# Optimization experiments

Measured on AMD Instinct MI355X. Metric: run time of the kernel, lower is better.

The kernel has to match this reference:

```python
import jax, jax.numpy as jnp
import numpy as np


def _cosine_alpha_bar(T, s=0.008):
    x = np.linspace(0.0, T, T + 1)
    ac = np.cos((x / T + s) / (1.0 + s) * np.pi / 2.0) ** 2
    ac = ac / ac[0]
    betas = np.clip(1.0 - ac[1:] / ac[:-1], 1e-5, 0.999)
    return jnp.asarray(np.cumprod(1.0 - betas), dtype=jnp.float32)


def setup_inputs():
    B, T, C, D, L, NS = 16, 1024, 16, 256, 4, 1000
    ks = list(jax.random.split(jax.random.key(0), 64))
    def w(i, shape, fan):
        return jax.random.normal(ks[i], shape, dtype=jnp.float32) / np.sqrt(fan)
    half = D // 2
    nf = half // 2
    inp = {}
    inp['x'] = jax.random.normal(ks[0], (B, T, C), dtype=jnp.float32)
    inp['t'] = jax.random.randint(ks[1], (B,), 0, NS, dtype=jnp.int32)
    dt = jax.random.uniform(ks[2], (B, T), minval=5e-4, maxval=2e-3, dtype=jnp.float32)
    inp['timestamps'] = jnp.cumsum(dt, axis=1)
    inp['mask'] = (jax.random.uniform(ks[3], (B, T, C)) > 0.3).astype(jnp.float32)
    inp['noise'] = jax.random.normal(ks[4], (B, T, D), dtype=jnp.float32)
    inp['n_heads'] = 4
    inp['alpha_bar'] = _cosine_alpha_bar(NS)
    inp['W_enc'] = w(5, (2 * C, D), 2 * C); inp['b_enc'] = jnp.zeros((D,), jnp.float32)
    inp['te_freqs'] = jnp.exp(-jnp.arange(half, dtype=jnp.float32) * np.log(10000.0) / half)
    inp['W_temb'] = w(6, (D, D), D); inp['b_temb'] = jnp.zeros((D,), jnp.float32)
    inp['th_a'] = 0.1 * jax.random.normal(ks[7], (half,), dtype=jnp.float32)
    inp['th_b'] = 0.1 * jax.random.normal(ks[8], (half,), dtype=jnp.float32)
    inp['th_freqs'] = (jnp.exp(-jnp.linspace(0.0, np.log(10000.0 / 4.0), nf)) * (2.0 * np.pi / 4.0)).astype(jnp.float32)
    inp['W_film'] = w(9, (D, 2 * D), D); inp['b_film'] = jnp.zeros((2 * D,), jnp.float32)
    inp['gru_Wih'] = w(10, (D, 3 * D), D); inp['gru_Whh'] = w(11, (D, 3 * D), D)
    inp['gru_bih'] = jnp.zeros((3 * D,), jnp.float32); inp['gru_bhh'] = jnp.zeros((3 * D,), jnp.float32)
    inp['ode_W1'] = w(12, (D, D), D); inp['ode_b1'] = jnp.zeros((D,), jnp.float32)
    inp['ode_W2'] = w(13, (D, D), D); inp['ode_b2'] = jnp.zeros((D,), jnp.float32)
    inp['tr_Wqkv'] = w(14, (L, D, 3 * D), D); inp['tr_bqkv'] = jnp.zeros((L, 3 * D), jnp.float32)
    inp['tr_Wo'] = w(15, (L, D, D), D); inp['tr_bo'] = jnp.zeros((L, D), jnp.float32)
    inp['tr_ln1_w'] = jnp.ones((L, D), jnp.float32); inp['tr_ln1_b'] = jnp.zeros((L, D), jnp.float32)
    inp['tr_ln2_w'] = jnp.ones((L, D), jnp.float32); inp['tr_ln2_b'] = jnp.zeros((L, D), jnp.float32)
    inp['tr_W1'] = w(16, (L, D, 4 * D), D); inp['tr_b1'] = jnp.zeros((L, 4 * D), jnp.float32)
    inp['tr_W2'] = w(17, (L, 4 * D, D), 4 * D); inp['tr_b2'] = jnp.zeros((L, D), jnp.float32)
    inp['trn_w'] = jnp.ones((D,), jnp.float32); inp['trn_b'] = jnp.zeros((D,), jnp.float32)
    return inp


def _ln(u, w_, b_):
    m = u.mean(-1, keepdims=True)
    v = u.var(-1, keepdims=True)
    return (u - m) / jnp.sqrt(v + 1e-5) * w_ + b_


def reference(x, t, timestamps, mask, noise, n_heads, alpha_bar, W_enc, b_enc, te_freqs, W_temb, b_temb, th_a, th_b, th_freqs, W_film, b_film, gru_Wih, gru_Whh, gru_bih, gru_bhh, ode_W1, ode_b1, ode_W2, ode_b2, tr_Wqkv, tr_bqkv, tr_Wo, tr_bo, tr_ln1_w, tr_ln1_b, tr_ln2_w, tr_ln2_b, tr_W1, tr_b1, tr_W2, tr_b2, trn_w, trn_b):
    B, T, C = x.shape
    D = W_enc.shape[1]
    hd = D // n_heads
    # latent encode + forward diffusion
    z = jax.nn.relu(jnp.concatenate([x, mask], -1) @ W_enc + b_enc)  # (B,T,D)
    ab = alpha_bar[t][:, None, None]
    h = jnp.sqrt(ab) * z + jnp.sqrt(1.0 - ab) * noise
    # diffusion-step sinusoidal embedding
    targ = t.astype(jnp.float32)[:, None] * te_freqs[None, :]
    te = (jnp.concatenate([jnp.sin(targ), jnp.cos(targ)], -1) @ W_temb + b_temb)[:, None, :]
    # TimeHybridEncoding: odd dims ramp, even dims interleaved sin/cos
    ts = timestamps
    ramp = ts[..., None] * th_a + th_b                       # (B,T,D/2)
    phase = ts[..., None] * th_freqs                         # (B,T,D/4)
    sc = jnp.stack([jnp.sin(phase), jnp.cos(phase)], -1).reshape(B, T, -1)
    tm = jnp.zeros((B, T, D), x.dtype).at[..., 0::2].set(sc).at[..., 1::2].set(ramp)
    gamma, beta = jnp.split(jax.nn.silu(te) @ W_film + b_film, 2, -1)
    tm = (1.0 + gamma) * tm + beta
    h = h + te + tm
    # Jump-ODE encoder: RK4 between events + GRUCell jump, as a scan
    dts = jnp.concatenate([jnp.zeros((B, 1), x.dtype), ts[:, 1:] - ts[:, :-1]], 1)[..., None]  # (B,T,1); dt0=0 -> identity ODE step
    def odef(hh):
        return jnp.tanh(hh @ ode_W1 + ode_b1) @ ode_W2 + ode_b2
    def step(hh, inp):
        xt, dt = inp
        f1 = odef(hh)
        f2 = odef(hh + 0.5 * dt * f1)
        f3 = odef(hh + 0.5 * dt * f2)
        f4 = odef(hh + dt * f3)
        hh = hh + dt / 6.0 * (f1 + 2.0 * f2 + 2.0 * f3 + f4)
        gi = xt @ gru_Wih + gru_bih
        gh = hh @ gru_Whh + gru_bhh
        ir, iz, inn = jnp.split(gi, 3, -1)
        hr, hz, hn = jnp.split(gh, 3, -1)
        r = jax.nn.sigmoid(ir + hr)
        zg = jax.nn.sigmoid(iz + hz)
        n = jnp.tanh(inn + r * hn)
        hh = (1.0 - zg) * n + zg * hh
        return hh, hh
    _, Hs = jax.lax.scan(step, jnp.zeros((B, D), x.dtype), (jnp.swapaxes(h, 0, 1), jnp.swapaxes(dts, 0, 1)))
    Hseq = jnp.swapaxes(Hs, 0, 1)  # (B,T,D)
    # pre-norm causal transformer encoder (eval mode, relu FFN), final LayerNorm
    causal = jnp.triu(jnp.full((T, T), -jnp.inf, dtype=x.dtype), 1)
    Ht = Hseq
    for l in range(tr_Wqkv.shape[0]):
        u = _ln(Ht, tr_ln1_w[l], tr_ln1_b[l])
        q, k, v = jnp.split(u @ tr_Wqkv[l] + tr_bqkv[l], 3, -1)
        q = q.reshape(B, T, n_heads, hd).transpose(0, 2, 1, 3)
        k = k.reshape(B, T, n_heads, hd).transpose(0, 2, 1, 3)
        v = v.reshape(B, T, n_heads, hd).transpose(0, 2, 1, 3)
        att = jax.nn.softmax(jnp.einsum('bhqd,bhkd->bhqk', q, k) / np.sqrt(hd) + causal, axis=-1)
        o = jnp.einsum('bhqk,bhkd->bhqd', att, v).transpose(0, 2, 1, 3).reshape(B, T, D)
        Ht = Ht + o @ tr_Wo[l] + tr_bo[l]
        u2 = _ln(Ht, tr_ln2_w[l], tr_ln2_b[l])
        Ht = Ht + jax.nn.relu(u2 @ tr_W1[l] + tr_b1[l]) @ tr_W2[l] + tr_b2[l]
    Ht = _ln(Ht, trn_w, trn_b)
    return Hseq + Ht
```

## Files before the change

kernel.cpp:

```cpp
#include <hip/hip_runtime.h>

#define Bz  16
#define Tz  1024
#define Cz  16
#define Dz  256
#define NHz 4
#define HDz 64
#define Lz  4
#define MROWS (Bz*Tz)
#define QB  8

__device__ __forceinline__ float sigmoidf_(float x){ return 1.0f/(1.0f+__expf(-x)); }
__device__ __forceinline__ float tanh_(float x){
  float e = __expf(2.f*x);
  return 1.f - 2.f/(e + 1.f);
}

__device__ __forceinline__ float dot2f(uint a, uint b, float c){
  float d;
  asm("v_dot2_f32_f16 %0, %1, %2, %3" : "=v"(d) : "v"(a), "v"(b), "v"(c));
  return d;
}
__device__ __forceinline__ uint f2h2(float a, float b){
  union { _Float16 h[2]; uint u; } r;
  r.h[0] = (_Float16)a; r.h[1] = (_Float16)b;
  return r.u;
}

__device__ __forceinline__ float red8(float a){
  int x = __builtin_amdgcn_update_dpp(0, __float_as_int(a), 0xB1, 0xF, 0xF, true);
  a += __int_as_float(x);
  x = __builtin_amdgcn_update_dpp(0, __float_as_int(a), 0x4E, 0xF, 0xF, true);
  a += __int_as_float(x);
  a += __shfl_xor(a, 4);
  return a;
}

__global__ __launch_bounds__(256) void k_prep(
    const float* __restrict__ W1, const float* __restrict__ W2, const float* __restrict__ Whh,
    uint* __restrict__ W1L, uint* __restrict__ W2L, uint* __restrict__ WhL)
{
  int m = blockIdx.x*256 + threadIdx.x;
  if (m < 65536){
    const float* W = (m < 32768) ? W1 : W2;
    uint* out = (m < 32768) ? W1L : W2L;
    int mm = m & 32767;
    int q = mm >> 2, cc = mm & 3;
    int i = q >> 9, l = q & 511;
    int j4 = l >> 3, ks = l & 7;
    int kp = ks*16 + i;
    int c = j4*4 + cc;
    out[mm] = f2h2(W[(2*kp)*256 + c], W[(2*kp+1)*256 + c]);
  } else if (m < 65536 + 98304){
    int mm = m - 65536;
    int g = mm >> 15;
    int r = mm & 32767;
    int q = r >> 2, cc = r & 3;
    int i = q >> 9, l = q & 511;
    int j4 = l >> 3, ks = l & 7;
    int kp = ks*16 + i;
    int c = j4*4 + cc;
    WhL[mm] = f2h2(Whh[(2*kp)*768 + g*256 + c], Whh[(2*kp+1)*768 + g*256 + c]);
  }
}

__global__ __launch_bounds__(256) void k_batch_emb(
    const int* __restrict__ t, const float* __restrict__ te_freqs,
    const float* __restrict__ W_temb, const float* __restrict__ b_temb,
    const float* __restrict__ W_film, const float* __restrict__ b_film,
    float* __restrict__ te_out, float* __restrict__ gamma_out, float* __restrict__ beta_out)
{
  int b = blockIdx.x; int j = threadIdx.x;
  __shared__ float s[256];
  __shared__ float ste[256];
  float tf = (float)t[b];
  if (j < 128){
    float targ = tf * te_freqs[j];
    s[j]     = __sinf(targ);
    s[j+128] = __cosf(targ);
  }
  __syncthreads();
  float a0=0,a1=0,a2=0,a3=0;
  #pragma unroll 8
  for (int k=0;k<256;k+=4){
    a0 = fmaf(s[k+0], W_temb[(k+0)*256+j], a0);
    a1 = fmaf(s[k+1], W_temb[(k+1)*256+j], a1);
    a2 = fmaf(s[k+2], W_temb[(k+2)*256+j], a2);
    a3 = fmaf(s[k+3], W_temb[(k+3)*256+j], a3);
  }
  float te = (a0+a1)+(a2+a3) + b_temb[j];
  te_out[b*256+j] = te;
  ste[j] = te * sigmoidf_(te);
  __syncthreads();
  float g0=0,g1=0,h0=0,h1=0;
  #pragma unroll 8
  for (int k=0;k<256;k+=2){
    float v0 = ste[k+0], v1 = ste[k+1];
    g0 = fmaf(v0, W_film[(k+0)*512+j],     g0);
    g1 = fmaf(v1, W_film[(k+1)*512+j],     g1);
    h0 = fmaf(v0, W_film[(k+0)*512+256+j], h0);
    h1 = fmaf(v1, W_film[(k+1)*512+256+j], h1);
  }
  gamma_out[b*256+j] = g0+g1 + b_film[j];
  beta_out [b*256+j] = h0+h1 + b_film[256+j];
}

__global__ __launch_bounds__(256) void k_encode(
    const float* __restrict__ x, const float* __restrict__ mask, const float* __restrict__ noise,
    const int* __restrict__ t, const float* __restrict__ alpha_bar, const float* __restrict__ ts,
    const float* __restrict__ W_enc, const float* __restrict__ b_enc,
    const float* __restrict__ th_a, const float* __restrict__ th_b, const float* __restrict__ th_freqs,
    const float* __restrict__ te, const float* __restrict__ gamma, const float* __restrict__ beta,
    float* __restrict__ H0)
{
  int bt = blockIdx.x; int b = bt >> 10;
  int j = threadIdx.x;
  __shared__ float in[32];
  if (j < 16)      in[j] = x[bt*16 + j];
  else if (j < 32) in[j] = mask[bt*16 + (j-16)];
  __syncthreads();
  float acc = 0.f;
  #pragma unroll
  for (int k=0;k<32;k++) acc = fmaf(in[k], W_enc[k*256+j], acc);
  float z = fmaxf(acc + b_enc[j], 0.f);
  float ab = alpha_bar[t[b]];
  float h = sqrtf(ab)*z + sqrtf(1.f-ab)*noise[(size_t)bt*256 + j];
  float tsv = ts[bt];
  float tm;
  if (j & 1){
    int i = (j-1) >> 1;
    tm = fmaf(tsv, th_a[i], th_b[i]);
  } else {
    int m = j >> 2;
    float ph = tsv * th_freqs[m];
    tm = ((j & 3) == 0) ? __sinf(ph) : __cosf(ph);
  }
  tm = fmaf(1.f + gamma[b*256+j], tm, beta[b*256+j]);
  H0[(size_t)bt*256 + j] = h + te[b*256+j] + tm;
}

template<bool RELU, bool RES>
__global__ __launch_bounds__(256) void k_gemm(
    const float* __restrict__ A, const float* __restrict__ W,
    const float* __restrict__ bias, const float* __restrict__ Rp,
    float* __restrict__ Cp, int M, int N, int K)
{
  __shared__ float As[16][68];
  __shared__ float Bs[16][64];
  int bn = blockIdx.x * 64, bm = blockIdx.y * 64;
  int tid = threadIdx.x;
  int tx = tid & 15, ty = tid >> 4;
  float acc[4][4] = {};
  for (int k0=0; k0<K; k0+=16){
    #pragma unroll
    for (int i=0;i<4;i++){
      int idx = tid + i*256;
      int m = idx >> 4, kk = idx & 15;
      As[kk][m] = A[(size_t)(bm+m)*K + k0+kk];
    }
    #pragma unroll
    for (int i=0;i<4;i++){
      int idx = tid + i*256;
      int kk = idx >> 6, n = idx & 63;
      Bs[kk][n] = W[(size_t)(k0+kk)*N + bn+n];
    }
    __syncthreads();
    #pragma unroll
    for (int kk=0;kk<16;kk++){
      float a0=As[kk][ty*4+0], a1=As[kk][ty*4+1], a2=As[kk][ty*4+2], a3=As[kk][ty*4+3];
      float b0=Bs[kk][tx*4+0], b1=Bs[kk][tx*4+1], b2=Bs[kk][tx*4+2], b3=Bs[kk][tx*4+3];
      acc[0][0]=fmaf(a0,b0,acc[0][0]); acc[0][1]=fmaf(a0,b1,acc[0][1]); acc[0][2]=fmaf(a0,b2,acc[0][2]); acc[0][3]=fmaf(a0,b3,acc[0][3]);
      acc[1][0]=fmaf(a1,b0,acc[1][0]); acc[1][1]=fmaf(a1,b1,acc[1][1]); acc[1][2]=fmaf(a1,b2,acc[1][2]); acc[1][3]=fmaf(a1,b3,acc[1][3]);
      acc[2][0]=fmaf(a2,b0,acc[2][0]); acc[2][1]=fmaf(a2,b1,acc[2][1]); acc[2][2]=fmaf(a2,b2,acc[2][2]); acc[2][3]=fmaf(a2,b3,acc[2][3]);
      acc[3][0]=fmaf(a3,b0,acc[3][0]); acc[3][1]=fmaf(a3,b1,acc[3][1]); acc[3][2]=fmaf(a3,b2,acc[3][2]); acc[3][3]=fmaf(a3,b3,acc[3][3]);
    }
    __syncthreads();
  }
  #pragma unroll
  for (int i=0;i<4;i++){
    int row = bm + ty*4 + i;
    #pragma unroll
    for (int jj=0;jj<4;jj++){
      int col = bn + tx*4 + jj;
      float v = acc[i][jj] + bias[col];
      if (RELU) v = fmaxf(v, 0.f);
      if (RES)  v += Rp[(size_t)row*N + col];
      Cp[(size_t)row*N + col] = v;
    }
  }
}

#define SCAN_LDS_BYTES (131072 + 1280)

#define DOT4V(WV, VW) { uint4 _w = (WV); \
  a0 = dot2f(_w.x, VW, a0); a1 = dot2f(_w.y, VW, a1); \
  a2 = dot2f(_w.z, VW, a2); a3 = dot2f(_w.w, VW, a3); }

#define MV16L(VB) { \
  uint4 q0=(VB)[ks5+0], q1=(VB)[ks5+1], q2=(VB)[ks5+2], q3=(VB)[ks5+3]; \
  DOT4V(w1s[0*512+tid], q0.x)  DOT4V(w1s[1*512+tid], q0.y)  DOT4V(w1s[2*512+tid], q0.z)  DOT4V(w1s[3*512+tid], q0.w)  \
  DOT4V(w1s[4*512+tid], q1.x)  DOT4V(w1s[5*512+tid], q1.y)  DOT4V(w1s[6*512+tid], q1.z)  DOT4V(w1s[7*512+tid], q1.w)  \
  DOT4V(w1s[8*512+tid], q2.x)  DOT4V(w1s[9*512+tid], q2.y)  DOT4V(w1s[10*512+tid], q2.z) DOT4V(w1s[11*512+tid], q2.w) \
  DOT4V(w1s[12*512+tid], q3.x) DOT4V(w1s[13*512+tid], q3.y) DOT4V(w1s[14*512+tid], q3.z) DOT4V(w1s[15*512+tid], q3.w) }

#define MV16R(W, VB) { \
  uint4 q0=(VB)[ks5+0], q1=(VB)[ks5+1], q2=(VB)[ks5+2], q3=(VB)[ks5+3]; \
  DOT4V(W[0], q0.x)  DOT4V(W[1], q0.y)  DOT4V(W[2], q0.z)  DOT4V(W[3], q0.w)  \
  DOT4V(W[4], q1.x)  DOT4V(W[5], q1.y)  DOT4V(W[6], q1.z)  DOT4V(W[7], q1.w)  \
  DOT4V(W[8], q2.x)  DOT4V(W[9], q2.y)  DOT4V(W[10], q2.z) DOT4V(W[11], q2.w) \
  DOT4V(W[12], q3.x) DOT4V(W[13], q3.y) DOT4V(W[14], q3.z) DOT4V(W[15], q3.w) }

#define DOTG(WV, VV, g0,g1,g2,g3) \
  g0 = dot2f((WV).x, VV, g0); g1 = dot2f((WV).y, VV, g1); \
  g2 = dot2f((WV).z, VV, g2); g3 = dot2f((WV).w, VV, g3);

#define LDQ(BUF, PO, I0) { \
  BUF[0]=WhL4[(PO)+((I0)+0)*512+tid]; BUF[1]=WhL4[(PO)+((I0)+1)*512+tid]; \
  BUF[2]=WhL4[(PO)+((I0)+2)*512+tid]; BUF[3]=WhL4[(PO)+((I0)+3)*512+tid]; }

#define DOTQ(BUF, Q, g0,g1,g2,g3) { \
  DOTG(BUF[0], (Q).x, g0,g1,g2,g3) DOTG(BUF[1], (Q).y, g0,g1,g2,g3) \
  DOTG(BUF[2], (Q).z, g0,g1,g2,g3) DOTG(BUF[3], (Q).w, g0,g1,g2,g3) }

__global__ __launch_bounds__(512) void k_scan(
    const uint* __restrict__ W1Lg, const uint* __restrict__ W2Lg, const uint* __restrict__ WhLg,
    const float* __restrict__ GI, const float* __restrict__ ts,
    const float* __restrict__ b1, const float* __restrict__ b2,
    const float* __restrict__ bhh, float* __restrict__ Hseq, float* __restrict__ Ht)
{
  extern __shared__ __align__(16) char smem[];
  uint4* w1s = (uint4*)smem;
  uint*  v2  = (uint*)(smem + 131072);
  const int b = blockIdx.x, tid = threadIdx.x;
  const int j4 = tid >> 3, ks = tid & 7;
  const int ks5 = ks*5;
  const uint4* W1L4 = (const uint4*)W1Lg;
  const uint4* W2L4 = (const uint4*)W2Lg;
  const uint4* WhL4 = (const uint4*)WhLg;
  #pragma unroll
  for (int i=0;i<16;i++) w1s[i*512+tid] = W1L4[i*512+tid];
  uint4 w2r[16];
  #pragma unroll
  for (int i=0;i<16;i++) w2r[i] = W2L4[i*512 + tid];
  if (tid < 320) v2[tid] = 0u;
  const float4 b1v  = ((const float4*)b1)[j4];
  const float4 b2v  = ((const float4*)b2)[j4];
  const float4 bhrv = ((const float4*)bhh)[j4];
  const float4 bhzv = ((const float4*)bhh)[64 + j4];
  const float4 bhnv = ((const float4*)bhh)[128 + j4];
  const float* tsb = ts + b*Tz;
  const float* gib = GI + (size_t)b*Tz*768;
  float* hsq = Hseq + (size_t)b*Tz*256;
  float* htp = Ht   + (size_t)b*Tz*256;
  const int wdw = 2*j4;
  const int wslot = (wdw >> 4)*20 + (wdw & 15);
  float4 h = {0.f,0.f,0.f,0.f};
  int cur = 0;
  float tsnext = tsb[0];
  float tprev = 0.f;
  __syncthreads();

  for (int tt=0; tt<Tz; ++tt){
    float tcur = tsnext;
    tsnext = tsb[(tt+1 < Tz) ? tt+1 : Tz-1];
    float dt = tcur - tprev; if (tt == 0) dt = 0.f;
    tprev = tcur;
    uint* bufA = v2 + (cur ? 160 : 0);
    uint* bufB = v2 + (cur ? 0 : 160);
    const uint4* vbA = (const uint4*)bufA;
    const uint4* vbB = (const uint4*)bufB;
    const float4 gi_r = *(const float4*)(gib + tt*768       + j4*4);
    const float4 gi_z = *(const float4*)(gib + tt*768 + 256 + j4*4);
    const float4 gi_n = *(const float4*)(gib + tt*768 + 512 + j4*4);
    uint4 whr[16];
    #pragma unroll
    for (int i=0;i<16;i++) whr[i] = WhL4[i*512 + tid];
    uint4 wA[4], wB[4];

    {
      float a0=0,a1=0,a2=0,a3=0;
      MV16L(vbA);
      a0=red8(a0); a1=red8(a1); a2=red8(a2); a3=red8(a3);
      float u0 = tanh_(a0+b1v.x), u1 = tanh_(a1+b1v.y);
      float u2 = tanh_(a2+b1v.z), u3 = tanh_(a3+b1v.w);
      if (ks == 0){
        uint2 pk; pk.x = f2h2(u0,u1); pk.y = f2h2(u2,u3);
        *(uint2*)(bufB + wslot) = pk;
      }
    }
    __syncthreads();
    float4 hn;
    LDQ(wA, 8192, 0)
    LDQ(wB, 8192, 4)
    {
      float a0=0,a1=0,a2=0,a3=0;
      MV16R(w2r, vbB);
      a0=red8(a0); a1=red8(a1); a2=red8(a2); a3=red8(a3);
      hn.x = fmaf(dt, a0+b2v.x, h.x);
      hn.y = fmaf(dt, a1+b2v.y, h.y);
      hn.z = fmaf(dt, a2+b2v.z, h.z);
      hn.w = fmaf(dt, a3+b2v.w, h.w);
      if (ks == 0){
        uint2 pk; pk.x = f2h2(hn.x,hn.y); pk.y = f2h2(hn.z,hn.w);
        *(uint2*)(bufA + wslot) = pk;
      }
    }
    __syncthreads();
    {
      uint4 q0=vbA[ks5+0], q1=vbA[ks5+1], q2=vbA[ks5+2], q3=vbA[ks5+3];
      float r0=0,r1=0,r2=0,r3=0, z0=0,z1=0,z2=0,z3=0, n0=0,n1=0,n2=0,n3=0;
      DOTG(whr[0], q0.x, r0,r1,r2,r3) DOTG(whr[1], q0.y, r0,r1,r2,r3)
      DOTG(whr[2], q0.z, r0,r1,r2,r3) DOTG(whr[3], q0.w, r0,r1,r2,r3)
      DOTG(whr[4], q1.x, r0,r1,r2,r3) DOTG(whr[5], q1.y, r0,r1,r2,r3)
      DOTG(whr[6], q1.z, r0,r1,r2,r3) DOTG(whr[7], q1.w, r0,r1,r2,r3)
      DOTG(whr[8], q2.x, r0,r1,r2,r3) DOTG(whr[9], q2.y, r0,r1,r2,r3)
      DOTG(whr[10],q2.z, r0,r1,r2,r3) DOTG(whr[11],q2.w, r0,r1,r2,r3)
      DOTG(whr[12],q3.x, r0,r1,r2,r3) DOTG(whr[13],q3.y, r0,r1,r2,r3)
      DOTG(whr[14],q3.z, r0,r1,r2,r3) DOTG(whr[15],q3.w, r0,r1,r2,r3)
      DOTQ(wA, q0, z0,z1,z2,z3)  LDQ(wA, 8192, 8)
      DOTQ(wB, q1, z0,z1,z2,z3)  LDQ(wB, 8192, 12)
      DOTQ(wA, q2, z0,z1,z2,z3)  LDQ(wA, 16384, 0)
      DOTQ(wB, q3, z0,z1,z2,z3)  LDQ(wB, 16384, 4)
      DOTQ(wA, q0, n0,n1,n2,n3)  LDQ(wA, 16384, 8)
      DOTQ(wB, q1, n0,n1,n2,n3)  LDQ(wB, 16384, 12)
      DOTQ(wA, q2, n0,n1,n2,n3)
      DOTQ(wB, q3, n0,n1,n2,n3)
      r0=red8(r0); r1=red8(r1); r2=red8(r2); r3=red8(r3);
      z0=red8(z0); z1=red8(z1); z2=red8(z2); z3=red8(z3);
      n0=red8(n0); n1=red8(n1); n2=red8(n2); n3=red8(n3);
      float gr0 = sigmoidf_(gi_r.x + r0 + bhrv.x);
      float gr1 = sigmoidf_(gi_r.y + r1 + bhrv.y);
      float gr2 = sigmoidf_(gi_r.z + r2 + bhrv.z);
      float gr3 = sigmoidf_(gi_r.w + r3 + bhrv.w);
      float gz0 = sigmoidf_(gi_z.x + z0 + bhzv.x);
      float gz1 = sigmoidf_(gi_z.y + z1 + bhzv.y);
      float gz2 = sigmoidf_(gi_z.z + z2 + bhzv.z);
      float gz3 = sigmoidf_(gi_z.w + z3 + bhzv.w);
      float gn0 = tanh_(gi_n.x + gr0*(n0 + bhnv.x));
      float gn1 = tanh_(gi_n.y + gr1*(n1 + bhnv.y));
      float gn2 = tanh_(gi_n.z + gr2*(n2 + bhnv.z));
      float gn3 = tanh_(gi_n.w + gr3*(n3 + bhnv.w));
      h.x = fmaf(gz0, hn.x - gn0, gn0);
      h.y = fmaf(gz1, hn.y - gn1, gn1);
      h.z = fmaf(gz2, hn.z - gn2, gn2);
      h.w = fmaf(gz3, hn.w - gn3, gn3);
      if (ks == 0){
        uint2 pk; pk.x = f2h2(h.x,h.y); pk.y = f2h2(h.z,h.w);
        *(uint2*)(bufB + wslot) = pk;
        *(float4*)(hsq + tt*256 + j4*4) = h;
        *(float4*)(htp + tt*256 + j4*4) = h;
      }
    }
    cur ^= 1;
    __syncthreads();
  }
}

__global__ __launch_bounds__(256) void k_attn(const float* __restrict__ QKV, float* __restrict__ O)
{
  int qb = blockIdx.x & (Tz/QB - 1);
  int bh = blockIdx.x / (Tz/QB);
  int b = bh >> 2, h = bh & 3;
  __shared__ uint Q2[QB][32];
  __shared__ float S[QB][Tz];
  __shared__ __align__(16) char kvbuf[64*68*4];
  __shared__ float rs[QB];
  uint  (*K2)[33] = (uint(*)[33])kvbuf;
  float (*Vs)[68] = (float(*)[68])kvbuf;
  int tid = threadIdx.x;
  const float* base = QKV + (size_t)b*Tz*768;
  for (int i = tid; i < QB*16; i += 256){
    int q = i >> 4, c = i & 15;
    const float4 v = *(const float4*)&base[(size_t)(qb*QB+q)*768 + h*64 + c*4];
    Q2[q][c*2]   = f2h2(v.x*0.125f, v.y*0.125f);
    Q2[q][c*2+1] = f2h2(v.z*0.125f, v.w*0.125f);
  }
  __syncthreads();
  int kmax = qb*QB + QB;
  int nkt = (kmax + 63) >> 6;
  int q = tid >> 5, i0 = tid & 31;
  int qg = qb*QB + q;
  for (int kt=0; kt<nkt; ++kt){
    for (int i=tid; i<64*16; i+=256){
      int r=i>>4, c=i&15;
      const float4 v = *(const float4*)&base[(size_t)(kt*64+r)*768 + 256 + h*64 + c*4];
      K2[r][c*2]   = f2h2(v.x, v.y);
      K2[r][c*2+1] = f2h2(v.z, v.w);
    }
    __syncthreads();
    float a0=0.f, a1=0.f;
    #pragma unroll 8
    for (int dp=0; dp<32; ++dp){
      uint qv = Q2[q][dp];
      a0 = dot2f(K2[i0][dp],    qv, a0);
      a1 = dot2f(K2[i0+32][dp], qv, a1);
    }
    int k0g = kt*64 + i0, k1g = k0g + 32;
    S[q][kt*64+i0]    = (k0g <= qg) ? a0 : -1e30f;
    S[q][kt*64+i0+32] = (k1g <= qg) ? a1 : -1e30f;
    __syncthreads();
  }
  int NK = nkt*64;
  float m = -1e30f;
  for (int kk=i0; kk<NK; kk+=32) m = fmaxf(m, S[q][kk]);
  #pragma unroll
  for (int o=16;o;o>>=1) m = fmaxf(m, __shfl_xor(m, o, 32));
  float sum = 0.f;
  for (int kk=i0; kk<NK; kk+=32){
    float p = __expf(S[q][kk] - m);
    S[q][kk] = p;
    sum += p;
  }
  #pragma unroll
  for (int o=16;o;o>>=1) sum += __shfl_xor(sum, o, 32);
  if (i0 == 0) rs[q] = 1.f/sum;
  int dq = tid & 15;
  int ks = (tid >> 4) & 1;
  float o0=0,o1=0,o2=0,o3=0;
  for (int kt=0; kt<nkt; ++kt){
    __syncthreads();
    for (int i=tid; i<64*16; i+=256){
      int r=i>>4, c=i&15;
      const float4 v = *(const float4*)&base[(size_t)(kt*64+r)*768 + 512 + h*64 + c*4];
      *(float4*)&Vs[r][c*4] = v;
    }
    __syncthreads();
    int kbase = kt*64;
    #pragma unroll 8
    for (int kk=ks; kk<64; kk+=2){
      float p = S[q][kbase+kk];
      const float4 vv = *(const float4*)&Vs[kk][dq*4];
      o0=fmaf(p,vv.x,o0); o1=fmaf(p,vv.y,o1); o2=fmaf(p,vv.z,o2); o3=fmaf(p,vv.w,o3);
    }
  }
  o0 += __shfl_xor(o0, 16); o1 += __shfl_xor(o1, 16);
  o2 += __shfl_xor(o2, 16); o3 += __shfl_xor(o3, 16);
  if (!(tid & 16)){
    float r = rs[q];
    size_t orow = ((size_t)b*Tz + qg)*256 + h*64 + dq*4;
    float4 ov = {o0*r, o1*r, o2*r, o3*r};
    *(float4*)&O[orow] = ov;
  }
}

template<bool FINAL>
__global__ __launch_bounds__(256) void k_ln(
    const float* __restrict__ in, const float* __restrict__ w, const float* __restrict__ bgain,
    const float* __restrict__ addv, float* __restrict__ out)
{
  int row  = blockIdx.x*4 + (threadIdx.x >> 6);
  int lane = threadIdx.x & 63;
  const float4 xv = ((const float4*)(in + (size_t)row*256))[lane];
  float s = xv.x + xv.y + xv.z + xv.w;
  #pragma unroll
  for (int o=32;o;o>>=1) s += __shfl_xor(s, o, 64);
  float mean = s * (1.f/256.f);
  float dx=xv.x-mean, dy=xv.y-mean, dz=xv.z-mean, dw=xv.w-mean;
  float qv = dx*dx + dy*dy + dz*dz + dw*dw;
  #pragma unroll
  for (int o=32;o;o>>=1) qv += __shfl_xor(qv, o, 64);
  float rstd = 1.f/sqrtf(qv*(1.f/256.f) + 1e-5f);
  const float4 wv = ((const float4*)w)[lane];
  const float4 bv = ((const float4*)bgain)[lane];
  float4 ov;
  ov.x = dx*rstd*wv.x + bv.x;
  ov.y = dy*rstd*wv.y + bv.y;
  ov.z = dz*rstd*wv.z + bv.z;
  ov.w = dw*rstd*wv.w + bv.w;
  if (FINAL){
    const float4 av = ((const float4*)(addv + (size_t)row*256))[lane];
    ov.x += av.x; ov.y += av.y; ov.z += av.z; ov.w += av.w;
  }
  ((float4*)(out + (size_t)row*256))[lane] = ov;
}

extern "C" void kernel_launch(void* const* d_in, const int* in_sizes, int n_in,
                              void* d_out, int out_size, void* d_ws, size_t ws_size,
                              hipStream_t stream)
{
  const float* x         = (const float*)d_in[0];
  const int*   t         = (const int*)  d_in[1];
  const float* ts        = (const float*)d_in[2];
  const float* mask      = (const float*)d_in[3];
  const float* noise     = (const float*)d_in[4];
  const float* alpha_bar = (const float*)d_in[6];
  const float* W_enc     = (const float*)d_in[7];
  const float* b_enc     = (const float*)d_in[8];
  const float* te_freqs  = (const float*)d_in[9];
  const float* W_temb    = (const float*)d_in[10];
  const float* b_temb    = (const float*)d_in[11];
  const float* th_a      = (const float*)d_in[12];
  const float* th_b      = (const float*)d_in[13];
  const float* th_freqs  = (const float*)d_in[14];
  const float* W_film    = (const float*)d_in[15];
  const float* b_film    = (const float*)d_in[16];
  const float* gru_Wih   = (const float*)d_in[17];
  const float* gru_Whh   = (const float*)d_in[18];
  const float* gru_bih   = (const float*)d_in[19];
  const float* gru_bhh   = (const float*)d_in[20];
  const float* ode_W1    = (const float*)d_in[21];
  const float* ode_b1    = (const float*)d_in[22];
  const float* ode_W2    = (const float*)d_in[23];
  const float* ode_b2    = (const float*)d_in[24];
  const float* tr_Wqkv   = (const float*)d_in[25];
  const float* tr_bqkv   = (const float*)d_in[26];
  const float* tr_Wo     = (const float*)d_in[27];
  const float* tr_bo     = (const float*)d_in[28];
  const float* tr_ln1_w  = (const float*)d_in[29];
  const float* tr_ln1_b  = (const float*)d_in[30];
  const float* tr_ln2_w  = (const float*)d_in[31];
  const float* tr_ln2_b  = (const float*)d_in[32];
  const float* tr_W1     = (const float*)d_in[33];
  const float* tr_b1     = (const float*)d_in[34];
  const float* tr_W2     = (const float*)d_in[35];
  const float* tr_b2     = (const float*)d_in[36];
  const float* trn_w     = (const float*)d_in[37];
  const float* trn_b     = (const float*)d_in[38];

  float* w = (float*)d_ws;
  float* te    = w;
  float* gamma = w + 4096;
  float* beta  = w + 8192;
  float* R1    = w + 12288;
  float* H0    = R1;
  float* GI    = R1 + 4*1024*1024;
  float* QKVb  = R1;
  float* F1    = R1;
  float* Hseq  = R1   + 16*1024*1024;
  float* Ht    = Hseq + 4*1024*1024;
  float* U     = Ht   + 4*1024*1024;
  float* O     = U    + 4*1024*1024;
  uint*  W1L   = (uint*)(O + 4*1024*1024);
  uint*  W2L   = W1L + 32768;
  uint*  WhL   = W2L + 32768;

  k_prep<<<640, 256, 0, stream>>>(ode_W1, ode_W2, gru_Whh, W1L, W2L, WhL);
  k_batch_emb<<<Bz, 256, 0, stream>>>(t, te_freqs, W_temb, b_temb, W_film, b_film, te, gamma, beta);
  k_encode<<<MROWS, 256, 0, stream>>>(x, mask, noise, t, alpha_bar, ts, W_enc, b_enc,
                                      th_a, th_b, th_freqs, te, gamma, beta, H0);
  k_gemm<false,false><<<dim3(768/64, MROWS/64), 256, 0, stream>>>(H0, gru_Wih, gru_bih, nullptr, GI, MROWS, 768, 256);

  hipFuncSetAttribute((const void*)k_scan, hipFuncAttributeMaxDynamicSharedMemorySize, SCAN_LDS_BYTES);
  k_scan<<<Bz, 512, SCAN_LDS_BYTES, stream>>>(W1L, W2L, WhL, GI, ts, ode_b1, ode_b2, gru_bhh, Hseq, Ht);

  for (int l=0; l<Lz; ++l){
    k_ln<false><<<MROWS/4, 256, 0, stream>>>(Ht, tr_ln1_w + l*256, tr_ln1_b + l*256, nullptr, U);
    k_gemm<false,false><<<dim3(768/64, MROWS/64), 256, 0, stream>>>(U, tr_Wqkv + (size_t)l*256*768, tr_bqkv + l*768, nullptr, QKVb, MROWS, 768, 256);
    k_attn<<<Bz*NHz*(Tz/QB), 256, 0, stream>>>(QKVb, O);
    k_gemm<false,true><<<dim3(256/64, MROWS/64), 256, 0, stream>>>(O, tr_Wo + (size_t)l*256*256, tr_bo + l*256, Ht, Ht, MROWS, 256, 256);
    k_ln<false><<<MROWS/4, 256, 0, stream>>>(Ht, tr_ln2_w + l*256, tr_ln2_b + l*256, nullptr, U);
    k_gemm<true,false><<<dim3(1024/64, MROWS/64), 256, 0, stream>>>(U, tr_W1 + (size_t)l*256*1024, tr_b1 + l*1024, nullptr, F1, MROWS, 1024, 256);
    k_gemm<false,true><<<dim3(256/64, MROWS/64), 256, 0, stream>>>(F1, tr_W2 + (size_t)l*1024*256, tr_b2 + l*256, Ht, Ht, MROWS, 256, 1024);
  }

  k_ln<true><<<MROWS/4, 256, 0, stream>>>(Ht, trn_w, trn_b, Hseq, (float*)d_out);
}
```

Before: 11.83 ms.

## Restructure GRU scan: DPP-only reduction, folded biases, earlier weight prefetch, drop Ht copy

Remaps the thread-to-(j4,ks) layout so the 8-lane reduction uses only DPP row operations instead of a cross-lane shuffle. It folds the r/z recurrent biases into the input-gate GEMM bias through a precomputed combined bias. The z and n weight loads are reissued earlier in larger batches to hide global latency behind the sync barriers. The scan no longer writes a duplicate Ht buffer, and the first transformer layer reads Hseq directly. The trade-off is higher register pressure, with launch bounds set to one block per CU.

```diff
diff --git a/kernel.cpp b/kernel.cpp
--- a/kernel.cpp
+++ b/kernel.cpp
@@ -32,13 +32,19 @@
   a += __int_as_float(x);
   x = __builtin_amdgcn_update_dpp(0, __float_as_int(a), 0x4E, 0xF, 0xF, true);
   a += __int_as_float(x);
-  a += __shfl_xor(a, 4);
+  x = __builtin_amdgcn_update_dpp(0, __float_as_int(a), 0x128, 0xF, 0xF, true);
+  a += __int_as_float(x);
   return a;
 }
+
+__device__ __forceinline__ int ks_of(int l){ return (l & 3) | ((l & 8) >> 1); }
+__device__ __forceinline__ int j4_of(int t){ return ((t & 4) >> 2) | ((t >> 4) << 1); }
 
 __global__ __launch_bounds__(256) void k_prep(
     const float* __restrict__ W1, const float* __restrict__ W2, const float* __restrict__ Whh,
-    uint* __restrict__ W1L, uint* __restrict__ W2L, uint* __restrict__ WhL)
+    const float* __restrict__ bih, const float* __restrict__ bhh,
+    uint* __restrict__ W1L, uint* __restrict__ W2L, uint* __restrict__ WhL,
+    float* __restrict__ biasC)
 {
   int m = blockIdx.x*256 + threadIdx.x;
   if (m < 65536){
@@ -47,7 +53,7 @@
     int mm = m & 32767;
     int q = mm >> 2, cc = mm & 3;
     int i = q >> 9, l = q & 511;
-    int j4 = l >> 3, ks = l & 7;
+    int ks = ks_of(l), j4 = j4_of(l);
     int kp = ks*16 + i;
     int c = j4*4 + cc;
     out[mm] = f2h2(W[(2*kp)*256 + c], W[(2*kp+1)*256 + c]);
@@ -57,10 +63,13 @@
     int r = mm & 32767;
     int q = r >> 2, cc = r & 3;
     int i = q >> 9, l = q & 511;
-    int j4 = l >> 3, ks = l & 7;
+    int ks = ks_of(l), j4 = j4_of(l);
     int kp = ks*16 + i;
     int c = j4*4 + cc;
     WhL[mm] = f2h2(Whh[(2*kp)*768 + g*256 + c], Whh[(2*kp+1)*768 + g*256 + c]);
+  } else if (m < 65536 + 98304 + 768){
+    int c = m - (65536 + 98304);
+    biasC[c] = bih[c] + ((c < 512) ? bhh[c] : 0.f);
   }
 }
 
@@ -214,25 +223,18 @@
   g0 = dot2f((WV).x, VV, g0); g1 = dot2f((WV).y, VV, g1); \
   g2 = dot2f((WV).z, VV, g2); g3 = dot2f((WV).w, VV, g3);
 
-#define LDQ(BUF, PO, I0) { \
-  BUF[0]=WhL4[(PO)+((I0)+0)*512+tid]; BUF[1]=WhL4[(PO)+((I0)+1)*512+tid]; \
-  BUF[2]=WhL4[(PO)+((I0)+2)*512+tid]; BUF[3]=WhL4[(PO)+((I0)+3)*512+tid]; }
-
-#define DOTQ(BUF, Q, g0,g1,g2,g3) { \
-  DOTG(BUF[0], (Q).x, g0,g1,g2,g3) DOTG(BUF[1], (Q).y, g0,g1,g2,g3) \
-  DOTG(BUF[2], (Q).z, g0,g1,g2,g3) DOTG(BUF[3], (Q).w, g0,g1,g2,g3) }
-
-__global__ __launch_bounds__(512) void k_scan(
+__global__ __launch_bounds__(512, 1) void k_scan(
     const uint* __restrict__ W1Lg, const uint* __restrict__ W2Lg, const uint* __restrict__ WhLg,
     const float* __restrict__ GI, const float* __restrict__ ts,
     const float* __restrict__ b1, const float* __restrict__ b2,
-    const float* __restrict__ bhh, float* __restrict__ Hseq, float* __restrict__ Ht)
+    const float* __restrict__ bhh, float* __restrict__ Hseq)
 {
   extern __shared__ __align__(16) char smem[];
   uint4* w1s = (uint4*)smem;
   uint*  v2  = (uint*)(smem + 131072);
   const int b = blockIdx.x, tid = threadIdx.x;
-  const int j4 = tid >> 3, ks = tid & 7;
+  const int ks = ks_of(tid & 63);
+  const int j4 = j4_of(tid);
   const int ks5 = ks*5;
   const uint4* W1L4 = (const uint4*)W1Lg;
   const uint4* W2L4 = (const uint4*)W2Lg;
@@ -245,37 +247,28 @@
   if (tid < 320) v2[tid] = 0u;
   const float4 b1v  = ((const float4*)b1)[j4];
   const float4 b2v  = ((const float4*)b2)[j4];
-  const float4 bhrv = ((const float4*)bhh)[j4];
-  const float4 bhzv = ((const float4*)bhh)[64 + j4];
   const float4 bhnv = ((const float4*)bhh)[128 + j4];
   const float* tsb = ts + b*Tz;
   const float* gib = GI + (size_t)b*Tz*768;
   float* hsq = Hseq + (size_t)b*Tz*256;
-  float* htp = Ht   + (size_t)b*Tz*256;
   const int wdw = 2*j4;
   const int wslot = (wdw >> 4)*20 + (wdw & 15);
   float4 h = {0.f,0.f,0.f,0.f};
   int cur = 0;
-  float tsnext = tsb[0];
   float tprev = 0.f;
   __syncthreads();
 
   for (int tt=0; tt<Tz; ++tt){
-    float tcur = tsnext;
-    tsnext = tsb[(tt+1 < Tz) ? tt+1 : Tz-1];
+    float tcur = tsb[tt];
     float dt = tcur - tprev; if (tt == 0) dt = 0.f;
     tprev = tcur;
     uint* bufA = v2 + (cur ? 160 : 0);
     uint* bufB = v2 + (cur ? 0 : 160);
     const uint4* vbA = (const uint4*)bufA;
     const uint4* vbB = (const uint4*)bufB;
-    const float4 gi_r = *(const float4*)(gib + tt*768       + j4*4);
-    const float4 gi_z = *(const float4*)(gib + tt*768 + 256 + j4*4);
-    const float4 gi_n = *(const float4*)(gib + tt*768 + 512 + j4*4);
     uint4 whr[16];
     #pragma unroll
     for (int i=0;i<16;i++) whr[i] = WhL4[i*512 + tid];
-    uint4 wA[4], wB[4];
 
     {
       float a0=0,a1=0,a2=0,a3=0;
@@ -288,10 +281,11 @@
         *(uint2*)(bufB + wslot) = pk;
       }
     }
+    uint4 wz1[8];
+    #pragma unroll
+    for (int i=0;i<8;i++) wz1[i] = WhL4[8192 + i*512 + tid];
     __syncthreads();
     float4 hn;
-    LDQ(wA, 8192, 0)
-    LDQ(wB, 8192, 4)
     {
       float a0=0,a1=0,a2=0,a3=0;
       MV16R(w2r, vbB);
@@ -305,10 +299,19 @@
         *(uint2*)(bufA + wslot) = pk;
       }
     }
+    uint4 wz2[8];
+    #pragma unroll
+    for (int i=0;i<8;i++) wz2[i] = WhL4[8192 + (8+i)*512 + tid];
+    const float4 gi_r = *(const float4*)(gib + tt*768       + j4*4);
+    const float4 gi_z = *(const float4*)(gib + tt*768 + 256 + j4*4);
+    const float4 gi_n = *(const float4*)(gib + tt*768 + 512 + j4*4);
     __syncthreads();
     {
       uint4 q0=vbA[ks5+0], q1=vbA[ks5+1], q2=vbA[ks5+2], q3=vbA[ks5+3];
       float r0=0,r1=0,r2=0,r3=0, z0=0,z1=0,z2=0,z3=0, n0=0,n1=0,n2=0,n3=0;
+      uint4 wn1[8];
+      #pragma unroll
+      for (int i=0;i<8;i++) wn1[i] = WhL4[16384 + i*512 + tid];
       DOTG(whr[0], q0.x, r0,r1,r2,r3) DOTG(whr[1], q0.y, r0,r1,r2,r3)
       DOTG(whr[2], q0.z, r0,r1,r2,r3) DOTG(whr[3], q0.w, r0,r1,r2,r3)
       DOTG(whr[4], q1.x, r0,r1,r2,r3) DOTG(whr[5], q1.y, r0,r1,r2,r3)
@@ -317,25 +320,36 @@
       DOTG(whr[10],q2.z, r0,r1,r2,r3) DOTG(whr[11],q2.w, r0,r1,r2,r3)
       DOTG(whr[12],q3.x, r0,r1,r2,r3) DOTG(whr[13],q3.y, r0,r1,r2,r3)
       DOTG(whr[14],q3.z, r0,r1,r2,r3) DOTG(whr[15],q3.w, r0,r1,r2,r3)
-      DOTQ(wA, q0, z0,z1,z2,z3)  LDQ(wA, 8192, 8)
-      DOTQ(wB, q1, z0,z1,z2,z3)  LDQ(wB, 8192, 12)
-      DOTQ(wA, q2, z0,z1,z2,z3)  LDQ(wA, 16384, 0)
-      DOTQ(wB, q3, z0,z1,z2,z3)  LDQ(wB, 16384, 4)
-      DOTQ(wA, q0, n0,n1,n2,n3)  LDQ(wA, 16384, 8)
-      DOTQ(wB, q1, n0,n1,n2,n3)  LDQ(wB, 16384, 12)
-      DOTQ(wA, q2, n0,n1,n2,n3)
-      DOTQ(wB, q3, n0,n1,n2,n3)
+      uint4 wn2[8];
+      #pragma unroll
+      for (int i=0;i<8;i++) wn2[i] = WhL4[16384 + (8+i)*512 + tid];
+      DOTG(wz1[0], q0.x, z0,z1,z2,z3) DOTG(wz1[1], q0.y, z0,z1,z2,z3)
+      DOTG(wz1[2], q0.z, z0,z1,z2,z3) DOTG(wz1[3], q0.w, z0,z1,z2,z3)
+      DOTG(wz1[4], q1.x, z0,z1,z2,z3) DOTG(wz1[5], q1.y, z0,z1,z2,z3)
+      DOTG(wz1[6], q1.z, z0,z1,z2,z3) DOTG(wz1[7], q1.w, z0,z1,z2,z3)
+      DOTG(wz2[0], q2.x, z0,z1,z2,z3) DOTG(wz2[1], q2.y, z0,z1,z2,z3)
+      DOTG(wz2[2], q2.z, z0,z1,z2,z3) DOTG(wz2[3], q2.w, z0,z1,z2,z3)
+      DOTG(wz2[4], q3.x, z0,z1,z2,z3) DOTG(wz2[5], q3.y, z0,z1,z2,z3)
+      DOTG(wz2[6], q3.z, z0,z1,z2,z3) DOTG(wz2[7], q3.w, z0,z1,z2,z3)
+      DOTG(wn1[0], q0.x, n0,n1,n2,n3) DOTG(wn1[1], q0.y, n0,n1,n2,n3)
+      DOTG(wn1[2], q0.z, n0,n1,n2,n3) DOTG(wn1[3], q0.w, n0,n1,n2,n3)
+      DOTG(wn1[4], q1.x, n0,n1,n2,n3) DOTG(wn1[5], q1.y, n0,n1,n2,n3)
+      DOTG(wn1[6], q1.z, n0,n1,n2,n3) DOTG(wn1[7], q1.w, n0,n1,n2,n3)
+      DOTG(wn2[0], q2.x, n0,n1,n2,n3) DOTG(wn2[1], q2.y, n0,n1,n2,n3)
+      DOTG(wn2[2], q2.z, n0,n1,n2,n3) DOTG(wn2[3], q2.w, n0,n1,n2,n3)
+      DOTG(wn2[4], q3.x, n0,n1,n2,n3) DOTG(wn2[5], q3.y, n0,n1,n2,n3)
+      DOTG(wn2[6], q3.z, n0,n1,n2,n3) DOTG(wn2[7], q3.w, n0,n1,n2,n3)
       r0=red8(r0); r1=red8(r1); r2=red8(r2); r3=red8(r3);
       z0=red8(z0); z1=red8(z1); z2=red8(z2); z3=red8(z3);
       n0=red8(n0); n1=red8(n1); n2=red8(n2); n3=red8(n3);
-      float gr0 = sigmoidf_(gi_r.x + r0 + bhrv.x);
-      float gr1 = sigmoidf_(gi_r.y + r1 + bhrv.y);
-      float gr2 = sigmoidf_(gi_r.z + r2 + bhrv.z);
-      float gr3 = sigmoidf_(gi_r.w + r3 + bhrv.w);
-      float gz0 = sigmoidf_(gi_z.x + z0 + bhzv.x);
-      float gz1 = sigmoidf_(gi_z.y + z1 + bhzv.y);
-      float gz2 = sigmoidf_(gi_z.z + z2 + bhzv.z);
-      float gz3 = sigmoidf_(gi_z.w + z3 + bhzv.w);
+      float gr0 = sigmoidf_(gi_r.x + r0);
+      float gr1 = sigmoidf_(gi_r.y + r1);
+      float gr2 = sigmoidf_(gi_r.z + r2);
+      float gr3 = sigmoidf_(gi_r.w + r3);
+      float gz0 = sigmoidf_(gi_z.x + z0);
+      float gz1 = sigmoidf_(gi_z.y + z1);
+      float gz2 = sigmoidf_(gi_z.z + z2);
+      float gz3 = sigmoidf_(gi_z.w + z3);
       float gn0 = tanh_(gi_n.x + gr0*(n0 + bhnv.x));
       float gn1 = tanh_(gi_n.y + gr1*(n1 + bhnv.y));
       float gn2 = tanh_(gi_n.z + gr2*(n2 + bhnv.z));
@@ -348,7 +362,6 @@
         uint2 pk; pk.x = f2h2(h.x,h.y); pk.y = f2h2(h.z,h.w);
         *(uint2*)(bufB + wslot) = pk;
         *(float4*)(hsq + tt*256 + j4*4) = h;
-        *(float4*)(htp + tt*256 + j4*4) = h;
       }
     }
     cur ^= 1;
@@ -533,21 +546,24 @@
   uint*  W1L   = (uint*)(O + 4*1024*1024);
   uint*  W2L   = W1L + 32768;
   uint*  WhL   = W2L + 32768;
-
-  k_prep<<<640, 256, 0, stream>>>(ode_W1, ode_W2, gru_Whh, W1L, W2L, WhL);
+  float* biasC = (float*)(WhL + 98304);
+
+  k_prep<<<643, 256, 0, stream>>>(ode_W1, ode_W2, gru_Whh, gru_bih, gru_bhh,
+                                  W1L, W2L, WhL, biasC);
   k_batch_emb<<<Bz, 256, 0, stream>>>(t, te_freqs, W_temb, b_temb, W_film, b_film, te, gamma, beta);
   k_encode<<<MROWS, 256, 0, stream>>>(x, mask, noise, t, alpha_bar, ts, W_enc, b_enc,
                                       th_a, th_b, th_freqs, te, gamma, beta, H0);
-  k_gemm<false,false><<<dim3(768/64, MROWS/64), 256, 0, stream>>>(H0, gru_Wih, gru_bih, nullptr, GI, MROWS, 768, 256);
+  k_gemm<false,false><<<dim3(768/64, MROWS/64), 256, 0, stream>>>(H0, gru_Wih, biasC, nullptr, GI, MROWS, 768, 256);
 
   hipFuncSetAttribute((const void*)k_scan, hipFuncAttributeMaxDynamicSharedMemorySize, SCAN_LDS_BYTES);
-  k_scan<<<Bz, 512, SCAN_LDS_BYTES, stream>>>(W1L, W2L, WhL, GI, ts, ode_b1, ode_b2, gru_bhh, Hseq, Ht);
+  k_scan<<<Bz, 512, SCAN_LDS_BYTES, stream>>>(W1L, W2L, WhL, GI, ts, ode_b1, ode_b2, gru_bhh, Hseq);
 
   for (int l=0; l<Lz; ++l){
-    k_ln<false><<<MROWS/4, 256, 0, stream>>>(Ht, tr_ln1_w + l*256, tr_ln1_b + l*256, nullptr, U);
+    const float* Hin = (l == 0) ? Hseq : Ht;
+    k_ln<false><<<MROWS/4, 256, 0, stream>>>(Hin, tr_ln1_w + l*256, tr_ln1_b + l*256, nullptr, U);
     k_gemm<false,false><<<dim3(768/64, MROWS/64), 256, 0, stream>>>(U, tr_Wqkv + (size_t)l*256*768, tr_bqkv + l*768, nullptr, QKVb, MROWS, 768, 256);
     k_attn<<<Bz*NHz*(Tz/QB), 256, 0, stream>>>(QKVb, O);
-    k_gemm<false,true><<<dim3(256/64, MROWS/64), 256, 0, stream>>>(O, tr_Wo + (size_t)l*256*256, tr_bo + l*256, Ht, Ht, MROWS, 256, 256);
+    k_gemm<false,true><<<dim3(256/64, MROWS/64), 256, 0, stream>>>(O, tr_Wo + (size_t)l*256*256, tr_bo + l*256, Hin, Ht, MROWS, 256, 256);
     k_ln<false><<<MROWS/4, 256, 0, stream>>>(Ht, tr_ln2_w + l*256, tr_ln2_b + l*256, nullptr, U);
     k_gemm<true,false><<<dim3(1024/64, MROWS/64), 256, 0, stream>>>(U, tr_W1 + (size_t)l*256*1024, tr_b1 + l*1024, nullptr, F1, MROWS, 1024, 256);
     k_gemm<false,true><<<dim3(256/64, MROWS/64), 256, 0, stream>>>(F1, tr_W2 + (size_t)l*1024*256, tr_b2 + l*256, Ht, Ht, MROWS, 256, 1024);
```

After: 13.00 ms. 1.1x slower.
